# Kernel tuning notes

Hardware: AMD Instinct MI355X
Metric: run time of the kernel (lower is better)

The kernel has to match this reference:

```python
import jax, jax.numpy as jnp
import numpy as np
import math

B, S, D = 4, 4096, 2048
HEAD_DIM = 128  # dim_model // head_nums = 2048 // 16
DEPTH = 12


def setup_inputs() -> dict:
    key = jax.random.key(0)
    ks = jax.random.split(key, 8)
    std = 0.1
    return {
        "x": jax.random.normal(ks[0], (B, S, D), dtype=jnp.float32),
        "WQ": jax.random.normal(ks[1], (D, 2 * HEAD_DIM), dtype=jnp.float32) * (D ** -0.5),
        "WK": jax.random.normal(ks[2], (D, 2 * HEAD_DIM), dtype=jnp.float32) * (D ** -0.5),
        "WV": jax.random.normal(ks[3], (D, 2 * HEAD_DIM), dtype=jnp.float32) * (D ** -0.5),
        "lambda_q1": jax.random.normal(ks[4], (HEAD_DIM,), dtype=jnp.float32) * std,
        "lambda_q2": jax.random.normal(ks[5], (HEAD_DIM,), dtype=jnp.float32) * std,
        "lambda_k1": jax.random.normal(ks[6], (HEAD_DIM,), dtype=jnp.float32) * std,
        "lambda_k2": jax.random.normal(ks[7], (HEAD_DIM,), dtype=jnp.float32) * std,
    }


def reference(x, WQ, WK, WV, lambda_q1, lambda_q2, lambda_k1, lambda_k2):
    scale = HEAD_DIM ** -0.5
    lambda_init = 0.8 - 0.6 * math.exp(-0.3 * DEPTH)

    q = x @ WQ                      # [B, S, 2*hd]
    k = x @ WK
    v = x @ WV                      # [B, S, 2*hd]
    q1, q2 = q[..., :HEAD_DIM], q[..., HEAD_DIM:]
    k1, k2 = k[..., :HEAD_DIM], k[..., HEAD_DIM:]

    a1 = jnp.einsum("bqd,bkd->bqk", q1, k1) * scale  # [B, S, S]
    a2 = jnp.einsum("bqd,bkd->bqk", q2, k2) * scale

    lambda_1 = jnp.exp(jnp.sum(lambda_q1 * lambda_k1))
    lambda_2 = jnp.exp(jnp.sum(lambda_q2 * lambda_k2))
    lam = lambda_1 + lambda_2 + lambda_init

    attn = jax.nn.softmax(a1, axis=-1) - lam * jax.nn.softmax(a2, axis=-1)
    return jnp.einsum("bqk,bkd->bqd", attn, v)  # [B, S, 2*hd]
```

## Files before the change

### kernel.cpp

```cpp
#include <hip/hip_runtime.h>
#include <stdint.h>

typedef unsigned short u16;
typedef __attribute__((ext_vector_type(4))) float f32x4;
typedef __attribute__((ext_vector_type(16))) float f32x16;
typedef __attribute__((ext_vector_type(8))) short s16x8;
typedef __attribute__((ext_vector_type(8))) __bf16 bf16x8;
typedef __attribute__((ext_vector_type(8))) unsigned short u16x8;
typedef __attribute__((ext_vector_type(4))) unsigned short u16x4;
typedef __attribute__((ext_vector_type(4))) uint32_t u32x4;
typedef __attribute__((ext_vector_type(2))) uint32_t u32x2;

__device__ __forceinline__ f32x4 mfma16(s16x8 a, s16x8 b, f32x4 c) {
  return __builtin_amdgcn_mfma_f32_16x16x32_bf16(
      __builtin_bit_cast(bf16x8, a), __builtin_bit_cast(bf16x8, b), c, 0, 0, 0);
}
__device__ __forceinline__ f32x16 mfma32(s16x8 a, s16x8 b, f32x16 c) {
  return __builtin_amdgcn_mfma_f32_32x32x16_bf16(
      __builtin_bit_cast(bf16x8, a), __builtin_bit_cast(bf16x8, b), c, 0, 0, 0);
}

__device__ __forceinline__ void gl_lds16(const u16* g, u16* l) {
  __builtin_amdgcn_global_load_lds(
      (const __attribute__((address_space(1))) void*)g,
      (__attribute__((address_space(3))) void*)l, 16, 0, 0);
}

__device__ __forceinline__ u16 bf16rne(float f) {
  uint32_t u = __builtin_bit_cast(uint32_t, f);
  u += 0x7fffu + ((u >> 16) & 1u);
  return (u16)(u >> 16);
}

__global__ void cast_w_kernel(const float* __restrict__ WQ, const float* __restrict__ WK,
                              const float* __restrict__ WV, u16* __restrict__ Wt, float qscale) {
  int i = blockIdx.x * 256 + threadIdx.x;
  int r = i >> 11, k = i & 2047;
  int sel = r >> 8, c = r & 255;
  const float* W = (sel == 0) ? WQ : (sel == 1) ? WK : WV;
  float v = W[(size_t)k * 256 + c];
  if (sel == 0) v *= qscale;
  Wt[i] = bf16rne(v);
}

__global__ __launch_bounds__(256) void proj_gemm(const float* __restrict__ x, const u16* __restrict__ Wt,
                                                 u16* __restrict__ Qb, u16* __restrict__ Kb,
                                                 u16* __restrict__ Vt) {
  const int bid = blockIdx.x;
  const int xcd = bid & 7, j = bid >> 3;
  const int m0 = (xcd * 16 + (j / 6)) * 128;
  const int n0 = (j % 6) * 128;
  const int tid = threadIdx.x, lane = tid & 63, w = tid >> 6;
  const int ln = lane & 15, quad = lane >> 4;
  const int wm = w & 1, wn = w >> 1;
  __shared__ __align__(16) u16 As[2][128 * 32];
  __shared__ __align__(16) u16 Bs[2][128 * 32];
  f32x4 acc[4][4];
#pragma unroll
  for (int i = 0; i < 4; ++i)
#pragma unroll
    for (int jj = 0; jj < 4; ++jj) acc[i][jj] = f32x4{0.f, 0.f, 0.f, 0.f};

  auto stageB = [&](int kk, int bi) {
#pragma unroll
    for (int i = 0; i < 2; ++i) {
      int p = tid + i * 256;
      int row = p >> 2, cg = (p & 3) ^ (row & 3);
      gl_lds16(Wt + (size_t)(n0 + row) * 2048 + kk + cg * 8, Bs[bi] + (size_t)(p - lane) * 8);
    }
  };

  f32x4 areg[2][2];
  auto loadA = [&](int kk) {
#pragma unroll
    for (int i = 0; i < 2; ++i) {
      int p = tid + i * 256;
      int row = p >> 2, cg = (p & 3) ^ (row & 3);
      const float* src = x + (size_t)(m0 + row) * 2048 + kk + cg * 8;
      areg[i][0] = *(const f32x4*)src;
      areg[i][1] = *(const f32x4*)(src + 4);
    }
  };
  auto writeA = [&](int bi) {
#pragma unroll
    for (int i = 0; i < 2; ++i) {
      int p = tid + i * 256;
      u16x8 o;
#pragma unroll
      for (int jj = 0; jj < 4; ++jj) {
        o[jj] = __builtin_bit_cast(u16, (__bf16)areg[i][0][jj]);
        o[4 + jj] = __builtin_bit_cast(u16, (__bf16)areg[i][1][jj]);
      }
      *(u16x8*)(As[bi] + (size_t)p * 8) = o;
    }
  };

  stageB(0, 0);
  loadA(0);
  writeA(0);

  for (int t = 0; t < 64; ++t) {
    __syncthreads();
    if (t + 1 < 64) {
      loadA((t + 1) * 32);
      stageB((t + 1) * 32, (t + 1) & 1);
    }
    const u16* Asb = As[t & 1];
    const u16* Bsb = Bs[t & 1];
    s16x8 a[4];
#pragma unroll
    for (int mt = 0; mt < 4; ++mt) {
      int r = wm * 64 + mt * 16 + ln;
      a[mt] = *(const s16x8*)(Asb + r * 32 + ((quad ^ (r & 3)) * 8));
    }
#pragma unroll
    for (int nt = 0; nt < 4; ++nt) {
      int r = wn * 64 + nt * 16 + ln;
      s16x8 bf = *(const s16x8*)(Bsb + r * 32 + ((quad ^ (r & 3)) * 8));
#pragma unroll
      for (int mt = 0; mt < 4; ++mt) acc[mt][nt] = mfma16(a[mt], bf, acc[mt][nt]);
    }
    if (t + 1 < 64) writeA((t + 1) & 1);
  }
#pragma unroll
  for (int mt = 0; mt < 4; ++mt)
#pragma unroll
    for (int nt = 0; nt < 4; ++nt) {
      int row0 = m0 + wm * 64 + mt * 16 + quad * 4;
      int col = n0 + wn * 64 + nt * 16 + ln;
      int sel = col >> 8, c = col & 255;
      u16x4 vv;
#pragma unroll
      for (int jj = 0; jj < 4; ++jj) vv[jj] = bf16rne(acc[mt][nt][jj]);
      if (sel == 2) {
        int b = row0 >> 12, s = row0 & 4095;
        *(u16x4*)(Vt + (size_t)b * 1048576 + (size_t)c * 4096 + s) = vv;
      } else {
        u16* dst = (sel == 0) ? Qb : Kb;
#pragma unroll
        for (int jj = 0; jj < 4; ++jj) dst[(size_t)(row0 + jj) * 256 + c] = vv[jj];
      }
    }
}

__global__ void lam_kernel(const float* __restrict__ lq1, const float* __restrict__ lq2,
                           const float* __restrict__ lk1, const float* __restrict__ lk2,
                           float* __restrict__ lamp) {
  int t = threadIdx.x;
  float d1 = lq1[t] * lk1[t] + lq1[t + 64] * lk1[t + 64];
  float d2 = lq2[t] * lk2[t] + lq2[t + 64] * lk2[t + 64];
#pragma unroll
  for (int off = 32; off; off >>= 1) {
    d1 += __shfl_xor(d1, off);
    d2 += __shfl_xor(d2, off);
  }
  if (t == 0) *lamp = expf(d1) + expf(d2) + (0.8f - 0.6f * expf(-3.6f));
}

__global__ __launch_bounds__(512, 2) void attn_kernel(const u16* __restrict__ Qb,
                                                      const u16* __restrict__ Kb,
                                                      const u16* __restrict__ Vt,
                                                      const float* __restrict__ lamp,
                                                      float* __restrict__ out) {
  const int bid = blockIdx.x;
  const int xcd = bid & 7;
  const int b = xcd >> 1;
  const int qt = ((bid >> 3) << 1) + (xcd & 1);
  const int tid = threadIdx.x, lane = tid & 63, w = tid >> 6;
  const int l5 = lane & 31, lh = lane >> 5;
  const int m = w & 1, kt = (w >> 1) & 1, qh = w >> 2;

  __shared__ __align__(16) char smem[134144];
  float* buf0 = (float*)smem;
  float* buf1 = (float*)(smem + 66560);
  float* ls = (float*)(smem + 133120);

  const u16* Kg0 = Kb + ((size_t)b * 4096) * 256;
  const u16* Vg0 = Vt + (size_t)b * 1048576;

  auto stage = [&](int kb, char* base) {
    u16* Ks = (u16*)base;
    u16* Vs = (u16*)(base + 32768);
#pragma unroll
    for (int i = 0; i < 4; ++i) {
      int p = tid + i * 512;
      int row = p >> 5, c = p & 31;
      int cg = (c & 16) | ((c ^ row) & 15);
      gl_lds16(Kg0 + (size_t)(kb + row) * 256 + cg * 8, Ks + (size_t)(p - lane) * 8);
    }
#pragma unroll
    for (int i = 0; i < 4; ++i) {
      int p = tid + i * 512;
      int row = p >> 3, c = p & 7;
      int cg = c ^ (row & 7);
      gl_lds16(Vg0 + (size_t)row * 4096 + kb + cg * 8, Vs + (size_t)(p - lane) * 8);
    }
  };

  stage(0, smem);

  s16x8 bq[8];
  {
    const u16* qp =
        Qb + ((size_t)(b * 4096 + qt * 64 + qh * 32 + l5)) * 256 + m * 128 + lh * 8;
#pragma unroll
    for (int s = 0; s < 8; ++s) bq[s] = *(const s16x8*)(qp + s * 16);
  }

  f32x16 O[8];
#pragma unroll
  for (int ct = 0; ct < 8; ++ct)
#pragma unroll
    for (int r = 0; r < 16; ++r) O[ct][r] = 0.f;
  float l_run = 0.f;

  for (int t = 0; t < 64; ++t) {
    __syncthreads();
    if (t + 1 < 64) stage((t + 1) * 64, smem + ((t + 1) & 1) * 65536);

    char* base = smem + (t & 1) * 65536;
    u16* Ks = (u16*)base;
    u16* Vs = (u16*)(base + 32768);

    f32x16 Sa, Sb;
#pragma unroll
    for (int r = 0; r < 16; ++r) { Sa[r] = 0.f; Sb[r] = 0.f; }
#pragma unroll
    for (int s = 0; s < 8; s += 2) {
      int row = kt * 32 + l5;
      int c0 = m * 16 + s * 2 + lh;
      int c1 = m * 16 + (s + 1) * 2 + lh;
      s16x8 a0 = *(const s16x8*)(Ks + row * 256 + (((c0 & 16) | ((c0 ^ row) & 15))) * 8);
      s16x8 a1 = *(const s16x8*)(Ks + row * 256 + (((c1 & 16) | ((c1 ^ row) & 15))) * 8);
      Sa = mfma32(a0, bq[s], Sa);
      Sb = mfma32(a1, bq[s + 1], Sb);
    }

    s16x8 vfr0[8], vfr1[8];
#pragma unroll
    for (int ct = 0; ct < 8; ++ct) {
      int row = ct * 32 + l5;
      int c0v = (kt * 32) / 8 + lh;
      int c1v = (kt * 32 + 16) / 8 + lh;
      vfr0[ct] = *(const s16x8*)(Vs + row * 64 + ((c0v ^ (row & 7)) * 8));
      vfr1[ct] = *(const s16x8*)(Vs + row * 64 + ((c1v ^ (row & 7)) * 8));
    }

    uint32_t P[8];
#pragma unroll
    for (int d = 0; d < 8; ++d) {
      float p0 = __builtin_amdgcn_exp2f(Sa[2 * d] + Sb[2 * d]);
      float p1 = __builtin_amdgcn_exp2f(Sa[2 * d + 1] + Sb[2 * d + 1]);
      l_run += p0 + p1;
      P[d] = (uint32_t)bf16rne(p0) | ((uint32_t)bf16rne(p1) << 16);
    }

#pragma unroll
    for (int ks = 0; ks < 2; ++ks) {
      u32x2 s02 = __builtin_amdgcn_permlane32_swap(P[ks * 4 + 0], P[ks * 4 + 2], false, false);
      u32x2 s13 = __builtin_amdgcn_permlane32_swap(P[ks * 4 + 1], P[ks * 4 + 3], false, false);
      u32x4 fd;
      fd[0] = s02[0]; fd[1] = s13[0]; fd[2] = s02[1]; fd[3] = s13[1];
      s16x8 pf = __builtin_bit_cast(s16x8, fd);
      if (ks == 0) {
#pragma unroll
        for (int ct = 0; ct < 8; ++ct) O[ct] = mfma32(vfr0[ct], pf, O[ct]);
      } else {
#pragma unroll
        for (int ct = 0; ct < 8; ++ct) O[ct] = mfma32(vfr1[ct], pf, O[ct]);
      }
    }
  }

  float lam = *lamp;
  l_run += __shfl_xor(l_run, 32);
  __syncthreads();
  if (lane < 32) ls[w * 32 + l5] = l_run;
  float* bufm = m ? buf1 : buf0;
  const int qb0 = qh * 32;
  if (kt == 1) {
#pragma unroll
    for (int ct = 0; ct < 8; ++ct)
#pragma unroll
      for (int r = 0; r < 16; ++r) {
        int vcol = ct * 32 + (r & 3) + 8 * (r >> 2) + 4 * lh;
        bufm[vcol * 65 + qb0 + l5] = O[ct][r];
      }
  }
  __syncthreads();
  if (kt == 0) {
    float linv = 1.f / (ls[w * 32 + l5] + ls[(w | 2) * 32 + l5]);
#pragma unroll
    for (int ct = 0; ct < 8; ++ct)
#pragma unroll
      for (int r = 0; r < 16; ++r) {
        int vcol = ct * 32 + (r & 3) + 8 * (r >> 2) + 4 * lh;
        bufm[vcol * 65 + qb0 + l5] = (O[ct][r] + bufm[vcol * 65 + qb0 + l5]) * linv;
      }
  }
  __syncthreads();
  float* og = out + ((size_t)(b * 4096 + qt * 64)) * 256;
  const int col = tid & 255, half = tid >> 8;
#pragma unroll
  for (int j2 = 0; j2 < 32; ++j2) {
    int q = half * 32 + j2;
    float v = buf0[col * 65 + q] - lam * buf1[col * 65 + q];
    og[(size_t)q * 256 + col] = v;
  }
}

extern "C" void kernel_launch(void* const* d_in, const int* in_sizes, int n_in,
                              void* d_out, int out_size, void* d_ws, size_t ws_size,
                              hipStream_t stream) {
  (void)in_sizes; (void)n_in; (void)out_size; (void)ws_size;
  const float* x   = (const float*)d_in[0];
  const float* WQ  = (const float*)d_in[1];
  const float* WK  = (const float*)d_in[2];
  const float* WV  = (const float*)d_in[3];
  const float* lq1 = (const float*)d_in[4];
  const float* lq2 = (const float*)d_in[5];
  const float* lk1 = (const float*)d_in[6];
  const float* lk2 = (const float*)d_in[7];
  float* out = (float*)d_out;

  char* ws = (char*)d_ws;
  u16* Wt = (u16*)ws;   ws += (size_t)768 * 2048 * 2;
  u16* Qb = (u16*)ws;   ws += (size_t)16384 * 256 * 2;
  u16* Kb = (u16*)ws;   ws += (size_t)16384 * 256 * 2;
  u16* Vt = (u16*)ws;   ws += (size_t)16384 * 256 * 2;
  float* lamp = (float*)ws;

  const float qscale = 0.0883883476f * 1.44269504f;

  hipLaunchKernelGGL(cast_w_kernel, dim3(6144), dim3(256), 0, stream, WQ, WK, WV, Wt, qscale);
  hipLaunchKernelGGL(proj_gemm, dim3(768), dim3(256), 0, stream, x, Wt, Qb, Kb, Vt);
  hipLaunchKernelGGL(lam_kernel, dim3(1), dim3(64), 0, stream, lq1, lq2, lk1, lk2, lamp);
  hipLaunchKernelGGL(attn_kernel, dim3(256), dim3(512), 0, stream, Qb, Kb, Vt, lamp, out);
}
```

Before: 405.1 us.

## Deepen QKV GEMM A-prefetch with two register buffers and manual waitcnt barriers

Restructures the projection GEMM main loop so the fp32 A tiles are loaded into alternating register sets two k-steps ahead. The loop is unrolled by two and uses an explicit s_waitcnt vmcnt(4) plus a raw s_barrier and sched_barrier in place of __syncthreads. The aim is to hide global-load latency for x behind the MFMA work instead of stalling each iteration. In exchange it uses more VGPRs, and it relies on a hand-counted vmcnt that must match the number of outstanding loads.

```diff
diff --git a/kernel.cpp b/kernel.cpp
--- a/kernel.cpp
+++ b/kernel.cpp
@@ -70,43 +70,33 @@
     }
   };
 
-  f32x4 areg[2][2];
-  auto loadA = [&](int kk) {
+  f32x4 aregE[2][2], aregO[2][2];
+  auto loadA = [&](f32x4 (&ar)[2][2], int kk) {
 #pragma unroll
     for (int i = 0; i < 2; ++i) {
       int p = tid + i * 256;
       int row = p >> 2, cg = (p & 3) ^ (row & 3);
       const float* src = x + (size_t)(m0 + row) * 2048 + kk + cg * 8;
-      areg[i][0] = *(const f32x4*)src;
-      areg[i][1] = *(const f32x4*)(src + 4);
-    }
-  };
-  auto writeA = [&](int bi) {
+      ar[i][0] = *(const f32x4*)src;
+      ar[i][1] = *(const f32x4*)(src + 4);
+    }
+  };
+  auto writeA = [&](int bi, f32x4 (&ar)[2][2]) {
 #pragma unroll
     for (int i = 0; i < 2; ++i) {
       int p = tid + i * 256;
       u16x8 o;
 #pragma unroll
       for (int jj = 0; jj < 4; ++jj) {
-        o[jj] = __builtin_bit_cast(u16, (__bf16)areg[i][0][jj]);
-        o[4 + jj] = __builtin_bit_cast(u16, (__bf16)areg[i][1][jj]);
+        o[jj] = __builtin_bit_cast(u16, (__bf16)ar[i][0][jj]);
+        o[4 + jj] = __builtin_bit_cast(u16, (__bf16)ar[i][1][jj]);
       }
       *(u16x8*)(As[bi] + (size_t)p * 8) = o;
     }
   };
-
-  stageB(0, 0);
-  loadA(0);
-  writeA(0);
-
-  for (int t = 0; t < 64; ++t) {
-    __syncthreads();
-    if (t + 1 < 64) {
-      loadA((t + 1) * 32);
-      stageB((t + 1) * 32, (t + 1) & 1);
-    }
-    const u16* Asb = As[t & 1];
-    const u16* Bsb = Bs[t & 1];
+  auto computeTile = [&](int bi) {
+    const u16* Asb = As[bi];
+    const u16* Bsb = Bs[bi];
     s16x8 a[4];
 #pragma unroll
     for (int mt = 0; mt < 4; ++mt) {
@@ -120,8 +110,40 @@
 #pragma unroll
       for (int mt = 0; mt < 4; ++mt) acc[mt][nt] = mfma16(a[mt], bf, acc[mt][nt]);
     }
-    if (t + 1 < 64) writeA((t + 1) & 1);
-  }
+  };
+
+  loadA(aregE, 0);
+  loadA(aregO, 32);
+  stageB(0, 0);
+  writeA(0, aregE);
+
+  for (int t = 0; t < 62; t += 2) {
+    asm volatile("s_waitcnt vmcnt(4) lgkmcnt(0)" ::: "memory");
+    __builtin_amdgcn_s_barrier();
+    __builtin_amdgcn_sched_barrier(0);
+    writeA(1, aregO);
+    stageB((t + 1) * 32, 1);
+    loadA(aregE, (t + 2) * 32);
+    computeTile(0);
+    asm volatile("s_waitcnt vmcnt(4) lgkmcnt(0)" ::: "memory");
+    __builtin_amdgcn_s_barrier();
+    __builtin_amdgcn_sched_barrier(0);
+    writeA(0, aregE);
+    stageB((t + 2) * 32, 0);
+    loadA(aregO, (t + 3) * 32);
+    computeTile(1);
+  }
+  asm volatile("s_waitcnt vmcnt(4) lgkmcnt(0)" ::: "memory");
+  __builtin_amdgcn_s_barrier();
+  __builtin_amdgcn_sched_barrier(0);
+  writeA(1, aregO);
+  stageB(63 * 32, 1);
+  computeTile(0);
+  asm volatile("s_waitcnt vmcnt(0) lgkmcnt(0)" ::: "memory");
+  __builtin_amdgcn_s_barrier();
+  __builtin_amdgcn_sched_barrier(0);
+  computeTile(1);
+
 #pragma unroll
   for (int mt = 0; mt < 4; ++mt)
 #pragma unroll
```

New measurement: 437.2 us. 7.9% more time.
